# Kernel tuning notes

Hardware: AMD Instinct MI355X
Metric: run time of the kernel (lower is better)

The kernel has to match this reference:

```python
import jax, jax.numpy as jnp
import numpy as np
import math

B, S, D = 2, 2048, 512
H = 8
DEPTH = D // H
MAX_REL = 1024
NEG_INF = -1.0e9


def skew(t):
    # t: (..., r, c). Pad a zero column on the left, reshape to move relative
    # logits into their absolute positions (Music Transformer skew trick).
    r, c = t.shape[-2], t.shape[-1]
    padded = jnp.pad(t, [(0, 0)] * (t.ndim - 1) + [(1, 0)])
    s = padded.reshape(-1, c + 1, r)[:, 1:]
    return s.reshape(t.shape)


def setup_inputs() -> dict:
    key = jax.random.key(0)
    ks = jax.random.split(key, 12)
    sc = 1.0 / math.sqrt(D)
    return {
        "q": jax.random.normal(ks[0], (B, S, D), jnp.float32),
        "k": jax.random.normal(ks[1], (B, S, D), jnp.float32),
        "v": jax.random.normal(ks[2], (B, S, D), jnp.float32),
        "mask": jax.random.randint(ks[3], (B, 1, S, S), 0, 2, jnp.int32),
        "Wq_w": jax.random.normal(ks[4], (D, D), jnp.float32) * sc,
        "Wq_b": jnp.zeros((D,), jnp.float32),
        "Wk_w": jax.random.normal(ks[5], (D, D), jnp.float32) * sc,
        "Wk_b": jnp.zeros((D,), jnp.float32),
        "Wv_w": jax.random.normal(ks[6], (D, D), jnp.float32) * sc,
        "Wv_b": jnp.zeros((D,), jnp.float32),
        "E": jax.random.normal(ks[7], (MAX_REL, D), jnp.float32),
        "Wo_w": jax.random.normal(ks[8], (D, D), jnp.float32) * sc,
        "Wo_b": jnp.zeros((D,), jnp.float32),
    }


def reference(q, k, v, mask, Wq_w, Wq_b, Wk_w, Wk_b, Wv_w, Wv_b, E, Wo_w, Wo_b):
    # Linear projections (torch Linear: x @ W^T + b)
    qp = q @ Wq_w.T + Wq_b
    kp = k @ Wk_w.T + Wk_b
    vp = v @ Wv_w.T + Wv_b

    # Required relative position embeddings for seq_len S (S >= MAX_REL here:
    # repeat E[0] for the first S-MAX_REL positions, then the full table).
    n_rep = max(0, S - MAX_REL)
    e = jnp.concatenate([jnp.tile(E[0:1], (n_rep, 1)), E[max(0, MAX_REL - S):]], axis=0)  # (S, D)

    # Split heads: (B,S,D)->(B,H,S,depth); e: (S,D)->(H,S,depth)
    qh = qp.reshape(B, S, H, DEPTH).transpose(0, 2, 1, 3)
    kh = kp.reshape(B, S, H, DEPTH).transpose(0, 2, 1, 3)
    vh = vp.reshape(B, S, H, DEPTH).transpose(0, 2, 1, 3)
    eh = e.reshape(S, H, DEPTH).transpose(1, 0, 2)

    QKt = jnp.einsum('bhqd,bhkd->bhqk', qh, kh)
    Srel = skew(jnp.einsum('bhqd,hkd->bhqk', qh, eh))
    logits = (QKt + Srel) / math.sqrt(DEPTH)
    logits = logits + mask.astype(logits.dtype) * NEG_INF
    attn = jnp.einsum('bhqk,bhkd->bhqd', jax.nn.softmax(logits, axis=-1), vh)

    # Merge heads and output projection
    out = attn.transpose(0, 2, 1, 3).reshape(B, S, D)
    return out @ Wo_w.T + Wo_b
```

## Files before the change

kernel.cpp:

```cpp
#include <hip/hip_runtime.h>
#include <hip/hip_bf16.h>

#define BB 2
#define SS 2048
#define DD 512
#define HH 8
#define DP 64
#define MR 1024

typedef __attribute__((ext_vector_type(8))) short bf16x8;
typedef __attribute__((ext_vector_type(4))) float floatx4;

static __device__ __forceinline__ unsigned short f2b(float x) {
    __hip_bfloat16 h = __float2bfloat16(x);
    return *reinterpret_cast<unsigned short*>(&h);
}
static __device__ __forceinline__ float b2f(unsigned short u) {
    __hip_bfloat16 h = *reinterpret_cast<__hip_bfloat16*>(&u);
    return __bfloat162float(h);
}
static __device__ __forceinline__ void gll16(const void* g, void* l) {
    __builtin_amdgcn_global_load_lds(
        (const __attribute__((address_space(1))) void*)g,
        (__attribute__((address_space(3))) void*)l, 16, 0, 0);
}
static __device__ __forceinline__ int xoff(int ks, int quad, int row) {
    return (((ks * 4 + quad) ^ (row & 7)) * 16);
}

__global__ __launch_bounds__(256) void prep_kernel(
    const float* __restrict__ Wq, const float* __restrict__ Wk,
    const float* __restrict__ Wv, const float* __restrict__ Wo,
    const float* __restrict__ E,  const float* __restrict__ q,
    const float* __restrict__ k,  const float* __restrict__ v,
    const int* __restrict__ mask,
    unsigned short* __restrict__ Wqb, unsigned short* __restrict__ Wkb,
    unsigned short* __restrict__ Wvb, unsigned short* __restrict__ Wob,
    unsigned short* __restrict__ Eb,  unsigned short* __restrict__ qb16,
    unsigned short* __restrict__ kb16, unsigned short* __restrict__ vb16,
    unsigned long long* __restrict__ bits)
{
    const int blk = blockIdx.x;
    if (blk < 7680) {
        const int gid = blk * 256 + threadIdx.x;
        const float* src; unsigned short* dst; int off;
        if      (gid < 65536)   { src = Wq; dst = Wqb;  off = gid; }
        else if (gid < 131072)  { src = Wk; dst = Wkb;  off = gid - 65536; }
        else if (gid < 196608)  { src = Wv; dst = Wvb;  off = gid - 131072; }
        else if (gid < 262144)  { src = Wo; dst = Wob;  off = gid - 196608; }
        else if (gid < 393216)  { src = E;  dst = Eb;   off = gid - 262144; }
        else if (gid < 917504)  { src = q;  dst = qb16; off = gid - 393216; }
        else if (gid < 1441792) { src = k;  dst = kb16; off = gid - 917504; }
        else                    { src = v;  dst = vb16; off = gid - 1441792; }
        float4 x = ((const float4*)src)[off];
        ushort4 u; u.x = f2b(x.x); u.y = f2b(x.y); u.z = f2b(x.z); u.w = f2b(x.w);
        ((ushort4*)dst)[off] = u;
    } else {
        const size_t wid = (size_t)(blk - 7680) * 4 + (threadIdx.x >> 6);
        const int lane = threadIdx.x & 63;
        const int mv = mask[wid * 64 + lane];
        unsigned long long bal = __ballot(mv != 0);
        if (lane == 0) bits[wid] = bal;
    }
}

__global__ __launch_bounds__(256) void gemm_proj(
    const unsigned short* __restrict__ Xq, const unsigned short* __restrict__ Xk,
    const unsigned short* __restrict__ Xv,
    const unsigned short* __restrict__ Wqb, const unsigned short* __restrict__ Wkb,
    const unsigned short* __restrict__ Wvb,
    const float* __restrict__ bq, const float* __restrict__ bk,
    const float* __restrict__ bv,
    const unsigned short* __restrict__ Eb,
    unsigned short* __restrict__ qp, unsigned short* __restrict__ kp,
    unsigned short* __restrict__ vpT, unsigned short* __restrict__ G)
{
    const int z = blockIdx.z;
    const unsigned short* A  = (z == 0) ? Xq : (z == 1) ? Xk : Xv;
    const unsigned short* Wb = (z == 0) ? Wqb : (z == 1) ? Wkb : Wvb;
    const float* bias        = (z == 0) ? bq : (z == 1) ? bk : bv;

    __shared__ __align__(16) char parena[27648];
    char* AsB = parena;
    char* WsB = parena + 8192;
    const int t = threadIdx.x, lane = t & 63, w = t >> 6;
    const int quad = lane >> 4, l15 = lane & 15;
    const int wm = w >> 1, wn = w & 1;
    const int m0 = blockIdx.x * 64, n0 = blockIdx.y * 64;

    int srow[2], scol[2];
#pragma unroll
    for (int i = 0; i < 2; i++) {
        const int p = (w * 2 + i) * 64 + lane;
        srow[i] = p >> 3; scol[i] = (p & 7) ^ (srow[i] & 7);
    }

    floatx4 acc[2][2];
#pragma unroll
    for (int mi = 0; mi < 2; mi++)
#pragma unroll
        for (int ni = 0; ni < 2; ni++)
            acc[mi][ni] = (floatx4){0.f, 0.f, 0.f, 0.f};

    for (int k0 = 0; k0 < 512; k0 += 64) {
        if (k0) __syncthreads();
#pragma unroll
        for (int i = 0; i < 2; i++) {
            gll16(A + (size_t)(m0 + srow[i]) * 512 + k0 + scol[i] * 8,
                  AsB + (w * 2 + i) * 1024);
            gll16(Wb + (size_t)(n0 + srow[i]) * 512 + k0 + scol[i] * 8,
                  WsB + (w * 2 + i) * 1024);
        }
        __syncthreads();
#pragma unroll
        for (int ks = 0; ks < 2; ks++) {
            bf16x8 a[2], bb[2];
#pragma unroll
            for (int mi = 0; mi < 2; mi++) {
                const int row = wm * 32 + mi * 16 + l15;
                a[mi] = *(const bf16x8*)(AsB + row * 128 + xoff(ks, quad, row));
            }
#pragma unroll
            for (int ni = 0; ni < 2; ni++) {
                const int row = wn * 32 + ni * 16 + l15;
                bb[ni] = *(const bf16x8*)(WsB + row * 128 + xoff(ks, quad, row));
            }
#pragma unroll
            for (int mi = 0; mi < 2; mi++)
#pragma unroll
                for (int ni = 0; ni < 2; ni++)
                    acc[mi][ni] = __builtin_amdgcn_mfma_f32_16x16x32_bf16(
                        a[mi], bb[ni], acc[mi][ni], 0, 0, 0);
        }
    }

    if (z == 1) {
#pragma unroll
        for (int ni = 0; ni < 2; ni++) {
            const int n = n0 + wn * 32 + ni * 16 + l15;
            const float bvl = bias[n];
#pragma unroll
            for (int mi = 0; mi < 2; mi++)
#pragma unroll
                for (int r = 0; r < 4; r++) {
                    const size_t m = (size_t)(m0 + wm * 32 + mi * 16 + quad * 4 + r);
                    kp[m * 512 + n] = f2b(acc[mi][ni][r] + bvl);
                }
        }
    } else if (z == 2) {
        __syncthreads();
        unsigned short* Ls = (unsigned short*)parena;
#pragma unroll
        for (int ni = 0; ni < 2; ni++) {
            const int dcol = wn * 32 + ni * 16 + l15;
            const float bvl = bias[n0 + dcol];
#pragma unroll
            for (int mi = 0; mi < 2; mi++)
#pragma unroll
                for (int r = 0; r < 4; r++) {
                    const int srw = wm * 32 + mi * 16 + quad * 4 + r;
                    Ls[dcol * 72 + srw] = f2b(acc[mi][ni][r] + bvl);
                }
        }
        __syncthreads();
        const int bb2 = blockIdx.x >> 5, s0 = (blockIdx.x & 31) * 64, hh = blockIdx.y;
        const int drow = t >> 2, sc8 = (t & 3) * 8;
#pragma unroll
        for (int half = 0; half < 2; half++) {
            *(uint4*)&vpT[((size_t)(bb2 * 8 + hh) * 64 + drow) * SS + s0 + half * 32 + sc8] =
                *(const uint4*)&Ls[drow * 72 + half * 32 + sc8];
        }
    } else {
        __syncthreads();
        unsigned short* Ls = (unsigned short*)parena;
#pragma unroll
        for (int ni = 0; ni < 2; ni++) {
            const int ch = wn * 32 + ni * 16 + l15;
            const float bvl = bias[n0 + ch];
#pragma unroll
            for (int mi = 0; mi < 2; mi++)
#pragma unroll
                for (int r = 0; r < 4; r++)
                    Ls[(wm * 32 + mi * 16 + quad * 4 + r) * 72 + ch] =
                        f2b(acc[mi][ni][r] + bvl);
        }
        __syncthreads();
        {
            const int row = t >> 2, c16 = (t & 3) * 16;
            const unsigned short* ls = &Ls[row * 72 + c16];
            unsigned short* qdst = &qp[(size_t)(m0 + row) * 512 + n0 + c16];
            *(uint4*)qdst = *(const uint4*)ls;
            *(uint4*)(qdst + 8) = *(const uint4*)(ls + 8);
        }
        bf16x8 af0 = *(const bf16x8*)&Ls[(w * 16 + l15) * 72 + quad * 8];
        bf16x8 af1 = *(const bf16x8*)&Ls[(w * 16 + l15) * 72 + 32 + quad * 8];

        const int bblk = m0 >> 11;
        const int i0 = m0 & 2047;
        const size_t grow0 = (size_t)(bblk * 8 + blockIdx.y) * SS + i0;
        char* EbL = parena + 10240;
        unsigned short* Gtw = (unsigned short*)(parena + 18432 + w * 2304);

        const int orow = lane >> 2, oseg = lane & 3;

        for (int tc = 0; tc < 16; tc++) {
            if (tc) __syncthreads();
#pragma unroll
            for (int i = 0; i < 2; i++)
                gll16(Eb + (size_t)(tc * 64 + srow[i]) * 512 + n0 + scol[i] * 8,
                      EbL + (w * 2 + i) * 1024);
            __syncthreads();
#pragma unroll
            for (int tt = 0; tt < 4; tt++) {
                const int row = tt * 16 + l15;
                bf16x8 b0 = *(const bf16x8*)(EbL + row * 128 + xoff(0, quad, row));
                bf16x8 b1 = *(const bf16x8*)(EbL + row * 128 + xoff(1, quad, row));
                floatx4 a2 = (floatx4){0.f, 0.f, 0.f, 0.f};
                a2 = __builtin_amdgcn_mfma_f32_16x16x32_bf16(af0, b0, a2, 0, 0, 0);
                a2 = __builtin_amdgcn_mfma_f32_16x16x32_bf16(af1, b1, a2, 0, 0, 0);
#pragma unroll
                for (int r = 0; r < 4; r++)
                    Gtw[(quad * 4 + r) * 72 + tt * 16 + l15] = f2b(a2[r]);
            }
            const unsigned short* gsrc = &Gtw[orow * 72 + oseg * 16];
            unsigned short* gdst = &G[(grow0 + w * 16 + orow) * MR + tc * 64 + oseg * 16];
            *(uint4*)gdst = *(const uint4*)gsrc;
            *(uint4*)(gdst + 8) = *(const uint4*)(gsrc + 8);
        }
    }
}

__global__ __launch_bounds__(256) void gemm_out(
    const unsigned short* __restrict__ A, const unsigned short* __restrict__ Wb,
    const float* __restrict__ bias, float* __restrict__ Out)
{
    __shared__ __align__(16) char parena[16384];
    char* AsB = parena;
    char* WsB = parena + 8192;
    const int t = threadIdx.x, lane = t & 63, w = t >> 6;
    const int quad = lane >> 4, l15 = lane & 15;
    const int wm = w >> 1, wn = w & 1;
    const int m0 = blockIdx.x * 64, n0 = blockIdx.y * 64;

    int srow[2], scol[2];
#pragma unroll
    for (int i = 0; i < 2; i++) {
        const int p = (w * 2 + i) * 64 + lane;
        srow[i] = p >> 3; scol[i] = (p & 7) ^ (srow[i] & 7);
    }

    floatx4 acc[2][2];
#pragma unroll
    for (int mi = 0; mi < 2; mi++)
#pragma unroll
        for (int ni = 0; ni < 2; ni++)
            acc[mi][ni] = (floatx4){0.f, 0.f, 0.f, 0.f};

    for (int k0 = 0; k0 < 512; k0 += 64) {
        if (k0) __syncthreads();
#pragma unroll
        for (int i = 0; i < 2; i++) {
            gll16(A + (size_t)(m0 + srow[i]) * 512 + k0 + scol[i] * 8,
                  AsB + (w * 2 + i) * 1024);
            gll16(Wb + (size_t)(n0 + srow[i]) * 512 + k0 + scol[i] * 8,
                  WsB + (w * 2 + i) * 1024);
        }
        __syncthreads();
#pragma unroll
        for (int ks = 0; ks < 2; ks++) {
            bf16x8 a[2], bb[2];
#pragma unroll
            for (int mi = 0; mi < 2; mi++) {
                const int row = wm * 32 + mi * 16 + l15;
                a[mi] = *(const bf16x8*)(AsB + row * 128 + xoff(ks, quad, row));
            }
#pragma unroll
            for (int ni = 0; ni < 2; ni++) {
                const int row = wn * 32 + ni * 16 + l15;
                bb[ni] = *(const bf16x8*)(WsB + row * 128 + xoff(ks, quad, row));
            }
#pragma unroll
            for (int mi = 0; mi < 2; mi++)
#pragma unroll
                for (int ni = 0; ni < 2; ni++)
                    acc[mi][ni] = __builtin_amdgcn_mfma_f32_16x16x32_bf16(
                        a[mi], bb[ni], acc[mi][ni], 0, 0, 0);
        }
    }
#pragma unroll
    for (int ni = 0; ni < 2; ni++) {
        const int n = n0 + wn * 32 + ni * 16 + l15;
        const float bvl = bias[n];
#pragma unroll
        for (int mi = 0; mi < 2; mi++)
#pragma unroll
            for (int r = 0; r < 4; r++) {
                const size_t m = (size_t)(m0 + wm * 32 + mi * 16 + quad * 4 + r);
                Out[m * 512 + n] = acc[mi][ni][r] + bvl;
            }
    }
}

struct RelPF { ushort4 hi; ushort4 lo; int path; };

static __device__ __forceinline__ void rel_issue(
    const unsigned short* __restrict__ pdiag, int i0w, int k0, int quad,
    RelPF pf[2])
{
#pragma unroll
    for (int ct = 0; ct < 2; ct++) {
        const int k0c = k0 + ct * 16;
        const int gj0 = k0c + quad * 4;
        const int dmax = i0w + 15 - k0c;
        const int dmin = i0w - (k0c + 15);
        int path;
        if (dmin >= MR) path = 0;
        else if (dmin >= 0 && dmax <= MR - 1) path = 1;
        else if (dmax <= -2 && dmin >= -(MR + 1)) path = 2;
        else if (dmax <= -(MR + 2)) path = 3;
        else path = 4;
        pf[ct].path = path;
        if (path == 1 || path == 4) {
            const unsigned short* p = pdiag + 1023 + gj0;
            pf[ct].hi.x = p[0]; pf[ct].hi.y = p[1];
            pf[ct].hi.z = p[2]; pf[ct].hi.w = p[3];
        }
        if (path == 3 || path == 4) {
            const unsigned short* p = pdiag + max(gj0 - 2, 0);
            pf[ct].lo.x = p[0]; pf[ct].lo.y = p[1];
            pf[ct].lo.z = p[2]; pf[ct].lo.w = p[3];
        }
    }
}

static __device__ __forceinline__ void rel_convert(
    const RelPF& pf, int gi, int k0c, int quad,
    float d0a, float d0b, float relc[4])
{
    const int path = pf.path;
    if (path == 0) {
        relc[0] = relc[1] = relc[2] = relc[3] = d0a;
    } else if (path == 1) {
        relc[0] = b2f(pf.hi.x); relc[1] = b2f(pf.hi.y);
        relc[2] = b2f(pf.hi.z); relc[3] = b2f(pf.hi.w);
    } else if (path == 2) {
        relc[0] = relc[1] = relc[2] = relc[3] = d0b;
    } else if (path == 3) {
        relc[0] = b2f(pf.lo.x); relc[1] = b2f(pf.lo.y);
        relc[2] = b2f(pf.lo.z); relc[3] = b2f(pf.lo.w);
    } else {
        const int gj0 = k0c + quad * 4;
        const unsigned short hv[4] = {pf.hi.x, pf.hi.y, pf.hi.z, pf.hi.w};
        const unsigned short lv[4] = {pf.lo.x, pf.lo.y, pf.lo.z, pf.lo.w};
#pragma unroll
        for (int r = 0; r < 4; r++) {
            const int dd = gi - (gj0 + r);
            float rl;
            if (dd >= MR) rl = d0a;
            else if (dd >= 0) rl = b2f(hv[r]);
            else if (dd == -1) rl = 0.0f;
            else if (dd >= -(MR + 1)) rl = d0b;
            else rl = b2f(lv[r]);
            relc[r] = rl;
        }
    }
}

__global__ __launch_bounds__(256, 4) void attn_kernel(
    const unsigned short* __restrict__ qp, const unsigned short* __restrict__ kp,
    const unsigned short* __restrict__ vpT, const unsigned int* __restrict__ mb32,
    const unsigned short* __restrict__ G, unsigned short* __restrict__ ao)
{
    __shared__ __align__(16) char smem[38016];
    const int t = threadIdx.x, lane = t & 63, w = t >> 6;
    const int quad = lane >> 4, l15 = lane & 15;
    const int wr = w >> 1, kh = w & 1;
    const int bh = blockIdx.y, b = bh >> 3, h = bh & 7;
    const int i0w = blockIdx.x * 32 + wr * 16;
    const int gi = i0w + l15;

    const unsigned short* kb = kp + (size_t)b * SS * DD + h * DP;
    const unsigned short* vb = vpT + (size_t)bh * DP * SS;
    const unsigned short* Gb = G + (size_t)bh * SS * MR;
    const unsigned int* mrow32 = mb32 + ((size_t)b * SS + gi) * 64;

    const unsigned short* qrow = qp + ((size_t)b * SS + gi) * DD + h * DP;
    bf16x8 qf0 = *(const bf16x8*)(qrow + quad * 8);
    bf16x8 qf1 = *(const bf16x8*)(qrow + 32 + quad * 8);

    const unsigned short* pdiag = Gb + (size_t)gi * 1023;
    const float d0a = b2f(Gb[(size_t)gi * MR]);
    const float d0b = b2f(Gb[(size_t)min(gi + 1, SS - 1) * MR]);

    char* Kh = smem + kh * 8192;
    char* Vh = smem + 16384 + kh * 8192;
    char* Pt = smem + 32768 + w * 1280;

    int kofs[2], vofs[2], dst[2];
#pragma unroll
    for (int i = 0; i < 2; i++) {
        const int c = wr * 2 + i;
        const int p = c * 64 + lane;
        const int krow = p >> 3, kcol = (p & 7) ^ (krow & 7);
        kofs[i] = krow * DD + kcol * 8;
        const int vrow = p >> 2, vcol = (p & 3) ^ (vrow & 3);
        vofs[i] = vrow * SS + vcol * 8;
        dst[i] = c * 1024;
    }

    floatx4 oacc[4];
#pragma unroll
    for (int ct = 0; ct < 4; ct++) oacc[ct] = (floatx4){0.f, 0.f, 0.f, 0.f};
    float lsum = 0.0f;

    {
        const int k0 = kh * 1024;
        gll16(kb + (size_t)k0 * DD + kofs[0], Kh + dst[0]);
        gll16(kb + (size_t)k0 * DD + kofs[1], Kh + dst[1]);
        gll16(vb + k0 + vofs[0], Vh + dst[0]);
        gll16(vb + k0 + vofs[1], Vh + dst[1]);
    }
    unsigned int mwv = mrow32[kh * 32];
    RelPF pf[2];
    rel_issue(pdiag, i0w, kh * 1024, quad, pf);

    const float C1 = 0.125f * 1.4426950408889634f;
    const float C2 = -18.75f * 1.4426950408889634f;

    for (int it = 0; it < 32; it++) {
        const int cur = it & 1;
        __syncthreads();
        if (it + 1 < 32) {
            const int k0n = kh * 1024 + (it + 1) * 32;
            const int nb = (cur ^ 1) * 4096;
            gll16(kb + (size_t)k0n * DD + kofs[0], Kh + nb + dst[0]);
            gll16(kb + (size_t)k0n * DD + kofs[1], Kh + nb + dst[1]);
            gll16(vb + k0n + vofs[0], Vh + nb + dst[0]);
            gll16(vb + k0n + vofs[1], Vh + nb + dst[1]);
        }
        const unsigned int mcur = mwv;

        float relc[2][4];
        rel_convert(pf[0], gi, kh * 1024 + it * 32,      quad, d0a, d0b, relc[0]);
        rel_convert(pf[1], gi, kh * 1024 + it * 32 + 16, quad, d0a, d0b, relc[1]);

        {
            const int itn = (it + 1 < 32) ? it + 1 : 31;
            mwv = mrow32[kh * 32 + itn];
            rel_issue(pdiag, i0w, kh * 1024 + itn * 32, quad, pf);
        }

        char* Kc = Kh + cur * 4096;
        char* Vc = Vh + cur * 4096;

        bf16x8 kf[2][2];
#pragma unroll
        for (int ct = 0; ct < 2; ct++) {
            const int row = ct * 16 + l15;
            kf[ct][0] = *(const bf16x8*)(Kc + row * 128 + ((quad ^ (l15 & 7)) * 16));
            kf[ct][1] = *(const bf16x8*)(Kc + row * 128 + (((4 + quad) ^ (l15 & 7)) * 16));
        }
        bf16x8 vf[4];
#pragma unroll
        for (int ct = 0; ct < 4; ct++) {
            const int drow = ct * 16 + l15;
            vf[ct] = *(const bf16x8*)(Vc + drow * 64 + ((quad ^ (drow & 3)) * 16));
        }

        floatx4 acc[2];
#pragma unroll
        for (int ct = 0; ct < 2; ct++) {
            const unsigned int nib = (mcur >> (ct * 16 + quad * 4)) & 0xFu;
            floatx4 a;
#pragma unroll
            for (int r = 0; r < 4; r++)
                a[r] = relc[ct][r] + (((nib >> r) & 1u) ? -8.0e9f : 0.0f);
            acc[ct] = a;
        }
        __builtin_amdgcn_s_setprio(1);
#pragma unroll
        for (int ct = 0; ct < 2; ct++) {
            acc[ct] = __builtin_amdgcn_mfma_f32_16x16x32_bf16(kf[ct][0], qf0, acc[ct], 0, 0, 0);
            acc[ct] = __builtin_amdgcn_mfma_f32_16x16x32_bf16(kf[ct][1], qf1, acc[ct], 0, 0, 0);
        }
        __builtin_amdgcn_s_setprio(0);

#pragma unroll
        for (int ct = 0; ct < 2; ct++) {
            const float p0 = __builtin_exp2f(fmaf(acc[ct][0], C1, C2));
            const float p1 = __builtin_exp2f(fmaf(acc[ct][1], C1, C2));
            const float p2 = __builtin_exp2f(fmaf(acc[ct][2], C1, C2));
            const float p3 = __builtin_exp2f(fmaf(acc[ct][3], C1, C2));
            lsum += (p0 + p1) + (p2 + p3);
            ushort4 u;
            u.x = f2b(p0); u.y = f2b(p1); u.z = f2b(p2); u.w = f2b(p3);
            *(ushort4*)(Pt + l15 * 80 + ct * 32 + quad * 8) = u;
        }

        bf16x8 pt = *(const bf16x8*)(Pt + l15 * 80 + quad * 16);
        __builtin_amdgcn_s_setprio(1);
#pragma unroll
        for (int ct = 0; ct < 4; ct++)
            oacc[ct] = __builtin_amdgcn_mfma_f32_16x16x32_bf16(vf[ct], pt, oacc[ct], 0, 0, 0);
        __builtin_amdgcn_s_setprio(0);
    }

    lsum += __shfl_xor(lsum, 16);
    lsum += __shfl_xor(lsum, 32);

    __syncthreads();
    float* OmW = (float*)(smem + wr * 4352);
    float* MlW = (float*)(smem + 37888);
    if (kh == 1) {
#pragma unroll
        for (int ct = 0; ct < 4; ct++)
            *(floatx4*)&OmW[l15 * 68 + ct * 16 + quad * 4] = oacc[ct];
        if (lane < 16) MlW[wr * 16 + lane] = lsum;
    }
    __syncthreads();
    if (kh == 0) {
        const float inv = 1.0f / (lsum + MlW[wr * 16 + l15]);
#pragma unroll
        for (int ct = 0; ct < 4; ct++) {
            floatx4 o1 = *(const floatx4*)&OmW[l15 * 68 + ct * 16 + quad * 4];
            ushort4 u;
            u.x = f2b((oacc[ct][0] + o1[0]) * inv);
            u.y = f2b((oacc[ct][1] + o1[1]) * inv);
            u.z = f2b((oacc[ct][2] + o1[2]) * inv);
            u.w = f2b((oacc[ct][3] + o1[3]) * inv);
            *(ushort4*)&ao[((size_t)b * SS + gi) * DD + h * DP + ct * 16 + quad * 4] = u;
        }
    }
}

extern "C" void kernel_launch(void* const* d_in, const int* in_sizes, int n_in,
                              void* d_out, int out_size, void* d_ws, size_t ws_size,
                              hipStream_t stream)
{
    const float* q    = (const float*)d_in[0];
    const float* k    = (const float*)d_in[1];
    const float* v    = (const float*)d_in[2];
    const int*   mask = (const int*)d_in[3];
    const float* Wq_w = (const float*)d_in[4];
    const float* Wq_b = (const float*)d_in[5];
    const float* Wk_w = (const float*)d_in[6];
    const float* Wk_b = (const float*)d_in[7];
    const float* Wv_w = (const float*)d_in[8];
    const float* Wv_b = (const float*)d_in[9];
    const float* E    = (const float*)d_in[10];
    const float* Wo_w = (const float*)d_in[11];
    const float* Wo_b = (const float*)d_in[12];
    float* out = (float*)d_out;

    char* ws = (char*)d_ws;
    unsigned short* G    = (unsigned short*)ws;
    unsigned short* qp   = (unsigned short*)(ws + 67108864);
    unsigned short* kp   = qp + 2097152;
    unsigned short* vpT  = kp + 2 * 2097152;
    unsigned short* qb16 = vpT + 2097152;
    unsigned short* kb16 = qb16 + 2097152;
    unsigned short* vb16 = kb16 + 2097152;
    unsigned short* aob  = qb16;
    unsigned long long* mbits = (unsigned long long*)(ws + 67108864 + 7 * 4194304);
    unsigned short* Wqb = (unsigned short*)(ws + 67108864 + 7 * 4194304 + 1048576);
    unsigned short* Wkb = Wqb + 262144;
    unsigned short* Wvb = Wkb + 262144;
    unsigned short* Wob = Wvb + 262144;
    unsigned short* Ebf = Wob + 262144;

    dim3 blk(256);
    hipLaunchKernelGGL(prep_kernel, dim3(40448), blk, 0, stream,
                       Wq_w, Wk_w, Wv_w, Wo_w, E, q, k, v, mask,
                       Wqb, Wkb, Wvb, Wob, Ebf, qb16, kb16, vb16, mbits);
    hipLaunchKernelGGL(gemm_proj, dim3(64, 8, 3), blk, 0, stream,
                       qb16, kb16, vb16, Wqb, Wkb, Wvb, Wq_b, Wk_b, Wv_b,
                       Ebf, qp, kp, vpT, G);
    hipLaunchKernelGGL(attn_kernel, dim3(64, 16), blk, 0, stream,
                       qp, kp, vpT, (const unsigned int*)mbits, G, aob);
    hipLaunchKernelGGL(gemm_out, dim3(64, 8), blk, 0, stream, aob, Wob, Wo_b, out);
}
```

Measured before the change: 224.8 us.

## Give each wave private K buffers, load V directly, drop block barrier

Each wave now stages its own K tile in LDS instead of splitting the work across wave pairs, which removes the per-iteration __syncthreads. V fragments are read straight from global memory into registers rather than staged through LDS. A manual s_waitcnt vmcnt(9) with a sched_barrier replaces the barrier for ordering. Softmax probabilities are packed to bf16 with v_cvt_pk_bf16_f32. The trade is redundant K loads per wave, more global traffic for V, and a hand-counted wait whose correctness depends on the exact number of outstanding loads.

```diff
diff --git a/kernel.cpp b/kernel.cpp
--- a/kernel.cpp
+++ b/kernel.cpp
@@ -18,6 +18,11 @@
 static __device__ __forceinline__ float b2f(unsigned short u) {
     __hip_bfloat16 h = *reinterpret_cast<__hip_bfloat16*>(&u);
     return __bfloat162float(h);
+}
+static __device__ __forceinline__ unsigned int cvtpk(float lo, float hi) {
+    unsigned int r;
+    asm("v_cvt_pk_bf16_f32 %0, %1, %2" : "=v"(r) : "v"(lo), "v"(hi));
+    return r;
 }
 static __device__ __forceinline__ void gll16(const void* g, void* l) {
     __builtin_amdgcn_global_load_lds(
@@ -392,20 +397,15 @@
     const float d0a = b2f(Gb[(size_t)gi * MR]);
     const float d0b = b2f(Gb[(size_t)min(gi + 1, SS - 1) * MR]);
 
-    char* Kh = smem + kh * 8192;
-    char* Vh = smem + 16384 + kh * 8192;
+    char* Kh = smem + w * 8192;
     char* Pt = smem + 32768 + w * 1280;
 
-    int kofs[2], vofs[2], dst[2];
-#pragma unroll
-    for (int i = 0; i < 2; i++) {
-        const int c = wr * 2 + i;
-        const int p = c * 64 + lane;
+    int kofs[4];
+#pragma unroll
+    for (int i = 0; i < 4; i++) {
+        const int p = i * 64 + lane;
         const int krow = p >> 3, kcol = (p & 7) ^ (krow & 7);
         kofs[i] = krow * DD + kcol * 8;
-        const int vrow = p >> 2, vcol = (p & 3) ^ (vrow & 3);
-        vofs[i] = vrow * SS + vcol * 8;
-        dst[i] = c * 1024;
     }
 
     floatx4 oacc[4];
@@ -413,13 +413,9 @@
     for (int ct = 0; ct < 4; ct++) oacc[ct] = (floatx4){0.f, 0.f, 0.f, 0.f};
     float lsum = 0.0f;
 
-    {
-        const int k0 = kh * 1024;
-        gll16(kb + (size_t)k0 * DD + kofs[0], Kh + dst[0]);
-        gll16(kb + (size_t)k0 * DD + kofs[1], Kh + dst[1]);
-        gll16(vb + k0 + vofs[0], Vh + dst[0]);
-        gll16(vb + k0 + vofs[1], Vh + dst[1]);
-    }
+#pragma unroll
+    for (int i = 0; i < 4; i++)
+        gll16(kb + (size_t)(kh * 1024) * DD + kofs[i], Kh + i * 1024);
     unsigned int mwv = mrow32[kh * 32];
     RelPF pf[2];
     rel_issue(pdiag, i0w, kh * 1024, quad, pf);
@@ -429,30 +425,26 @@
 
     for (int it = 0; it < 32; it++) {
         const int cur = it & 1;
-        __syncthreads();
+        const int k0 = kh * 1024 + it * 32;
+
         if (it + 1 < 32) {
-            const int k0n = kh * 1024 + (it + 1) * 32;
-            const int nb = (cur ^ 1) * 4096;
-            gll16(kb + (size_t)k0n * DD + kofs[0], Kh + nb + dst[0]);
-            gll16(kb + (size_t)k0n * DD + kofs[1], Kh + nb + dst[1]);
-            gll16(vb + k0n + vofs[0], Vh + nb + dst[0]);
-            gll16(vb + k0n + vofs[1], Vh + nb + dst[1]);
-        }
+            const size_t kro = (size_t)(k0 + 32) * DD;
+            char* nb = Kh + (cur ^ 1) * 4096;
+#pragma unroll
+            for (int i = 0; i < 4; i++)
+                gll16(kb + kro + kofs[i], nb + i * 1024);
+        }
+        bf16x8 vf[4];
+#pragma unroll
+        for (int ct = 0; ct < 4; ct++)
+            vf[ct] = *(const bf16x8*)(vb + (size_t)(ct * 16 + l15) * SS + k0 + quad * 8);
         const unsigned int mcur = mwv;
-
-        float relc[2][4];
-        rel_convert(pf[0], gi, kh * 1024 + it * 32,      quad, d0a, d0b, relc[0]);
-        rel_convert(pf[1], gi, kh * 1024 + it * 32 + 16, quad, d0a, d0b, relc[1]);
-
-        {
-            const int itn = (it + 1 < 32) ? it + 1 : 31;
-            mwv = mrow32[kh * 32 + itn];
-            rel_issue(pdiag, i0w, kh * 1024 + itn * 32, quad, pf);
-        }
+        mwv = mrow32[kh * 32 + ((it + 1 < 32) ? it + 1 : 31)];
+
+        asm volatile("s_waitcnt vmcnt(9)" ::: "memory");
+        __builtin_amdgcn_sched_barrier(0);
 
         char* Kc = Kh + cur * 4096;
-        char* Vc = Vh + cur * 4096;
-
         bf16x8 kf[2][2];
 #pragma unroll
         for (int ct = 0; ct < 2; ct++) {
@@ -460,11 +452,13 @@
             kf[ct][0] = *(const bf16x8*)(Kc + row * 128 + ((quad ^ (l15 & 7)) * 16));
             kf[ct][1] = *(const bf16x8*)(Kc + row * 128 + (((4 + quad) ^ (l15 & 7)) * 16));
         }
-        bf16x8 vf[4];
-#pragma unroll
-        for (int ct = 0; ct < 4; ct++) {
-            const int drow = ct * 16 + l15;
-            vf[ct] = *(const bf16x8*)(Vc + drow * 64 + ((quad ^ (drow & 3)) * 16));
+
+        float relc[2][4];
+        rel_convert(pf[0], gi, k0,      quad, d0a, d0b, relc[0]);
+        rel_convert(pf[1], gi, k0 + 16, quad, d0a, d0b, relc[1]);
+        {
+            const int itn = (it + 1 < 32) ? it + 1 : 31;
+            rel_issue(pdiag, i0w, kh * 1024 + itn * 32, quad, pf);
         }
 
         floatx4 acc[2];
@@ -492,9 +486,10 @@
             const float p2 = __builtin_exp2f(fmaf(acc[ct][2], C1, C2));
             const float p3 = __builtin_exp2f(fmaf(acc[ct][3], C1, C2));
             lsum += (p0 + p1) + (p2 + p3);
-            ushort4 u;
-            u.x = f2b(p0); u.y = f2b(p1); u.z = f2b(p2); u.w = f2b(p3);
-            *(ushort4*)(Pt + l15 * 80 + ct * 32 + quad * 8) = u;
+            uint2 u;
+            u.x = cvtpk(p0, p1);
+            u.y = cvtpk(p2, p3);
+            *(uint2*)(Pt + l15 * 80 + ct * 32 + quad * 8) = u;
         }
 
         bf16x8 pt = *(const bf16x8*)(Pt + l15 * 80 + quad * 16);
```

New measurement: 279.7 us. +24.4%, slower.
